# Kernel tuning notes

Hardware: AMD Instinct MI355X
Metric: run time of the kernel (lower is better)

The kernel has to match this reference:

```python
import jax, jax.numpy as jnp
import numpy as np

B, T, N, D = 2, 10, 1024, 1024
NH = 16
HD = D // NH


def setup_inputs() -> dict:
    key = jax.random.key(0)
    ks = jax.random.split(key, 9)
    data = jax.random.normal(ks[0], (B, N, D), jnp.float32)
    traj_pos = jax.random.normal(ks[1], (B, T, N, 3), jnp.float32)
    q = jax.random.normal(ks[2], (B, T, N, 4), jnp.float32)
    traj_quat = q / (jnp.linalg.norm(q, axis=-1, keepdims=True) + 1e-10)
    certainty = jax.random.uniform(ks[3], (B, N), jnp.float32)
    s = 1.0 / np.sqrt(D).astype(np.float32)
    Wq = jax.random.normal(ks[4], (D, D), jnp.float32) * s
    Wk = jax.random.normal(ks[5], (D, D), jnp.float32) * s
    Wv = jax.random.normal(ks[6], (D, D), jnp.float32) * s
    Wo = jax.random.normal(ks[7], (D, D), jnp.float32) * s
    z = jnp.zeros((D,), jnp.float32)
    return {"data": data, "traj_pos": traj_pos, "traj_quat": traj_quat,
            "certainty": certainty, "Wq": Wq, "bq": z, "Wk": Wk, "bk": z,
            "Wv": Wv, "bv": z, "Wo": Wo, "bo": z}


def reference(data, traj_pos, traj_quat, certainty, Wq, bq, Wk, bk, Wv, bv, Wo, bo):
    b, n, d = data.shape
    # --- trajectory similarity scores (same for all batches: torch.mean over batch+time) ---
    # pos_dist[i,j] = mean_{b,t} ||p_bti - p_btj||
    pd = jnp.linalg.norm(traj_pos[:, :, :, None, :] - traj_pos[:, :, None, :, :], axis=-1).mean(axis=(0, 1))  # (n,n)
    qdm = jnp.linalg.norm(traj_quat[:, :, :, None, :] - traj_quat[:, :, None, :, :], axis=-1).mean(axis=(0, 1))
    qdp = jnp.linalg.norm(traj_quat[:, :, :, None, :] + traj_quat[:, :, None, :, :], axis=-1).mean(axis=(0, 1))
    qd = jnp.minimum(qdm, qdp)
    traj = jnp.exp(-pd - qd)
    traj = traj / traj.sum(axis=-1, keepdims=True)  # (n,n) row-normalized

    def proj(x, W, bias):
        return (x @ W.T + bias).reshape(b, n, NH, HD).transpose(0, 2, 1, 3)  # (b,h,n,hd)

    Q = proj(data, Wq, bq)
    K = proj(data, Wk, bk)
    V = proj(data, Wv, bv)
    scores = jnp.einsum('bhid,bhjd->bhij', Q, K) / np.sqrt(HD).astype(np.float32)
    combined = scores + 0.5 * traj[None, None]  # broadcast over (batch, heads)
    attn = jax.nn.softmax(combined, axis=-1)
    out = jnp.einsum('bhij,bhjd->bhid', attn, V).transpose(0, 2, 1, 3).reshape(b, n, d)
    out = out @ Wo.T + bo
    # certainty update from attention entropy
    avg_attn = attn.mean(axis=1)  # (b,n,n)
    p = jnp.clip(avg_attn, 1e-10, None)
    Hent = -jnp.sum(p * jnp.log(p), axis=-1)  # (b,n)
    H_max = np.log(n).astype(np.float32)
    new_certainty = jnp.maximum(certainty, jax.nn.sigmoid(H_max - Hent))
    return out, new_certainty
```

## Files before the change

### kernel.cpp

```cpp
#include <hip/hip_runtime.h>
#include <math.h>

#define NB 2
#define NN 1024
#define DD 1024
#define NHH 16
#define HDD 64
#define BTT 20

typedef unsigned short u16;
typedef short bf16x8 __attribute__((ext_vector_type(8)));
typedef float f32x4 __attribute__((ext_vector_type(4)));

#define HMAXL 6.93147180559945f
#define C1 0.18033688011112042f
#define TLC 0.72134752044448170f
#define KC  0.072134752044448170f
#define CH 520

#define TRAJ_OFF 0
#define TL_OFF    1048576
#define DATAB_OFF 1572864
#define WQB_OFF   2621440
#define WKB_OFF   3145728
#define WVB_OFF   3670016
#define WOB_OFF   4194304
#define QB_OFF    4718592
#define KB_OFF    5767168
#define VT_OFF    6815744
#define AOB_OFF   7864320
#define LV_OFF    8912896
#define HPART_OFF 8945664
#define RSP_OFF   8978432

__device__ __forceinline__ float b2f(u16 h) { return __uint_as_float(((unsigned)h) << 16); }
__device__ __forceinline__ u16 f2bf(float f) {
  unsigned u = __float_as_uint(f);
  return (u16)((u + 0x7fffu + ((u >> 16) & 1u)) >> 16);
}
__device__ __forceinline__ void dma16(const void* g, void* l) {
  __builtin_amdgcn_global_load_lds((const __attribute__((address_space(1))) void*)g,
                                   (__attribute__((address_space(3))) void*)l, 16, 0, 0);
}

__global__ __launch_bounds__(256) void prep_kernel(const float* __restrict__ data,
                                                   const float* __restrict__ w0,
                                                   const float* __restrict__ w1,
                                                   const float* __restrict__ w2,
                                                   const float* __restrict__ w3,
                                                   u16* __restrict__ dd,
                                                   u16* __restrict__ d0, u16* __restrict__ d1,
                                                   u16* __restrict__ d2, u16* __restrict__ d3,
                                                   const float* __restrict__ pos,
                                                   const float* __restrict__ quat,
                                                   float* __restrict__ w,
                                                   float* __restrict__ rsp) {
  const int tid = threadIdx.x;
  const int bid = blockIdx.x;
  __shared__ float ld[8][BTT][8];
  __shared__ float wredS[4][8];
  if (bid >= 512) {
    int cb = bid - 512;
    int z = cb >> 10;
    const float* s;
    u16* d;
    size_t off = 0;
    if (z < 2) { s = data; d = dd; off = (size_t)z * 1048576; }
    else if (z == 2) { s = w0; d = d0; }
    else if (z == 3) { s = w1; d = d1; }
    else if (z == 4) { s = w2; d = d2; }
    else { s = w3; d = d3; }
    size_t i = off + (size_t)((cb & 1023) * 256 + tid) * 4;
    float4 v = *(const float4*)(s + i);
    ushort4 o = {f2bf(v.x), f2bf(v.y), f2bf(v.z), f2bf(v.w)};
    *(ushort4*)(d + i) = o;
    return;
  }
  const int jx = bid & 3;
  const int j = jx * 256 + tid;
  const int i0 = (bid >> 2) * 8;
  if (tid < 8 * BTT) {
    int ii = tid / BTT, bt = tid % BTT;
    const float* pp = pos + ((size_t)bt * NN + i0 + ii) * 3;
    ld[ii][bt][0] = pp[0]; ld[ii][bt][1] = pp[1]; ld[ii][bt][2] = pp[2];
    *(float4*)&ld[ii][bt][4] = *(const float4*)(quat + ((size_t)bt * NN + i0 + ii) * 4);
  }
  __syncthreads();
  float acc[8] = {};
  for (int bt = 0; bt < BTT; ++bt) {
    const float* pj = pos + ((size_t)bt * NN + j) * 3;
    float pjx = pj[0], pjy = pj[1], pjz = pj[2];
    float4 qj = *(const float4*)(quat + ((size_t)bt * NN + j) * 4);
#pragma unroll
    for (int ii = 0; ii < 8; ++ii) {
      float4 pi = *(const float4*)&ld[ii][bt][0];
      float4 qi = *(const float4*)&ld[ii][bt][4];
      float dx = pi.x - pjx, dy = pi.y - pjy, dz = pi.z - pjz;
      float d2 = fmaf(dz, dz, fmaf(dy, dy, dx * dx));
      float dot = fmaf(qi.w, qj.w, fmaf(qi.z, qj.z, fmaf(qi.y, qj.y, qi.x * qj.x)));
      float tq = fmaf(-2.f, fabsf(dot), 2.f);
      acc[ii] += sqrtf(d2) + sqrtf(fmaxf(tq, 0.f));
    }
  }
  const int wv = tid >> 6;
#pragma unroll
  for (int ii = 0; ii < 8; ++ii) {
    float v = exp2f(-acc[ii] * KC);
    w[(size_t)(i0 + ii) * NN + j] = v;
    float s = v;
#pragma unroll
    for (int off = 1; off < 64; off <<= 1) s += __shfl_xor(s, off, 64);
    if ((tid & 63) == 0) wredS[wv][ii] = s;
  }
  __syncthreads();
  if (tid < 8)
    rsp[jx * 1024 + i0 + tid] = wredS[0][tid] + wredS[1][tid] + wredS[2][tid] + wredS[3][tid];
}

__global__ __launch_bounds__(256) void qkv_trajB_kernel(const u16* __restrict__ Ab,
                                                        const u16* __restrict__ Wq,
                                                        const u16* __restrict__ Wk,
                                                        const u16* __restrict__ Wv,
                                                        const float* __restrict__ bq,
                                                        const float* __restrict__ bk,
                                                        const float* __restrict__ bv,
                                                        u16* __restrict__ Qb,
                                                        u16* __restrict__ Kb,
                                                        u16* __restrict__ VtT,
                                                        const float* __restrict__ wtr,
                                                        const float* __restrict__ rsp,
                                                        u16* __restrict__ tl) {
  const int tid = threadIdx.x;
  __shared__ __align__(16) u16 As[128 * 32];
  __shared__ __align__(16) u16 Bs[64 * 32];
  if (blockIdx.x < 256) {
    int base = blockIdx.x * 4;
#pragma unroll
    for (int r = 0; r < 4; ++r) {
      int i = base + r;
      float inv = TLC / (rsp[i] + rsp[1024 + i] + rsp[2048 + i] + rsp[3072 + i]);
      float4 w4 = *(const float4*)(wtr + (size_t)i * NN + tid * 4);
      ushort4 o = {f2bf(w4.x * inv), f2bf(w4.y * inv), f2bf(w4.z * inv), f2bf(w4.w * inv)};
      *(ushort4*)(tl + (size_t)i * NN + tid * 4) = o;
    }
    return;
  }
  const int bid = blockIdx.x - 256;
  const int z = bid >> 8;
  const int rem = bid & 255;
  const int bn = (rem & 15) << 6;
  const int bm = (rem >> 4) << 7;
  const u16* Wb = z == 0 ? Wq : (z == 1 ? Wk : Wv);
  const float* bias = z == 0 ? bq : (z == 1 ? bk : bv);
  const int w = tid >> 6, l = tid & 63, g = l >> 4, ln = l & 15;
  const int srow = w * 16 + (l >> 2);
  const int scol = (l & 3) * 8;
  const u16* Ap0 = Ab + (size_t)(bm + srow) * DD + scol;
  const u16* Ap1 = Ab + (size_t)(bm + 64 + srow) * DD + scol;
  const u16* Bp0 = Wb + (size_t)(bn + srow) * DD + scol;
  u16* dA0 = As + w * 512;
  u16* dA1 = As + 2048 + w * 512;
  u16* dB0 = Bs + w * 512;
  const int mw = (w & 1) * 64, nw = (w >> 1) * 32;
  f32x4 zero4 = {0.f, 0.f, 0.f, 0.f};
  f32x4 acc[4][2];
#pragma unroll
  for (int mt = 0; mt < 4; ++mt)
#pragma unroll
    for (int nt = 0; nt < 2; ++nt) acc[mt][nt] = zero4;
  for (int k0 = 0; k0 < DD; k0 += 32) {
    __syncthreads();
    dma16(Ap0 + k0, dA0); dma16(Ap1 + k0, dA1);
    dma16(Bp0 + k0, dB0);
    __syncthreads();
    bf16x8 bfr[2], afr[4];
#pragma unroll
    for (int nt = 0; nt < 2; ++nt)
      bfr[nt] = *(const bf16x8*)&Bs[(nw + nt * 16 + ln) * 32 + g * 8];
#pragma unroll
    for (int mt = 0; mt < 4; ++mt)
      afr[mt] = *(const bf16x8*)&As[(mw + mt * 16 + ln) * 32 + g * 8];
#pragma unroll
    for (int mt = 0; mt < 4; ++mt)
#pragma unroll
      for (int nt = 0; nt < 2; ++nt)
        acc[mt][nt] = __builtin_amdgcn_mfma_f32_16x16x32_bf16(afr[mt], bfr[nt], acc[mt][nt], 0, 0, 0);
  }
#pragma unroll
  for (int nt = 0; nt < 2; ++nt) {
    int n = bn + nw + nt * 16 + ln;
    float bb = bias[n];
    if (z == 2) {
      int row = (((bm >> 10) << 4) + (n >> 6)) * 64 + (n & 63);
#pragma unroll
      for (int mt = 0; mt < 4; ++mt) {
        int tok = (bm & 1023) + mw + mt * 16 + g * 4;
        ushort4 pk = {f2bf(acc[mt][nt][0] + bb), f2bf(acc[mt][nt][1] + bb),
                      f2bf(acc[mt][nt][2] + bb), f2bf(acc[mt][nt][3] + bb)};
        *(ushort4*)(VtT + (size_t)row * NN + tok) = pk;
      }
    } else {
      u16* outp = z == 0 ? Qb : Kb;
#pragma unroll
      for (int mt = 0; mt < 4; ++mt) {
#pragma unroll
        for (int r = 0; r < 4; ++r) {
          int m = bm + mw + mt * 16 + g * 4 + r;
          outp[(size_t)m * DD + n] = f2bf(acc[mt][nt][r] + bb);
        }
      }
    }
  }
}

__global__ __launch_bounds__(256) void att_kernel(const u16* __restrict__ Qb,
                                                  const u16* __restrict__ Kb,
                                                  const u16* __restrict__ VtT,
                                                  const u16* __restrict__ tl,
                                                  u16* __restrict__ AOb,
                                                  float* __restrict__ Lv) {
  const int tid = threadIdx.x;
  const int bh = blockIdx.y;
  const int b = bh >> 4, h = bh & 15;
  const int i0 = blockIdx.x << 6;
  const int w = tid >> 6, l = tid & 63, g = l >> 4, ln = l & 15;
  const int wi0 = w * 16;
  __shared__ __align__(16) u16 Qs[8 * CH];
  __shared__ __align__(16) u16 Ks[2][8 * CH];
  __shared__ __align__(16) u16 Vts[2][8 * CH];
  __shared__ __align__(16) u16 Pt[64 * 72];
  __shared__ float lsc[64];
  const int c0 = 2 * w, c1 = 2 * w + 1;
  const int rr = 8 * (l >> 3);
  const int dcol = (l & 7) * 8;
  dma16(Qb + ((size_t)(b * NN) + i0 + c0 + rr) * DD + h * HDD + dcol, Qs + c0 * CH);
  dma16(Qb + ((size_t)(b * NN) + i0 + c1 + rr) * DD + h * HDD + dcol, Qs + c1 * CH);
  const int ig = i0 + wi0 + ln;
  const int lnlo = (ln & 7) * CH;
  const int lnhi = (ln >> 3) * 64;
  f32x4 zero4 = {0.f, 0.f, 0.f, 0.f};
  f32x4 oacc[4];
#pragma unroll
  for (int nt = 0; nt < 4; ++nt) oacc[nt] = zero4;
  float lacc = 0.f;
  for (int j0 = 0; j0 < NN; j0 += 128) {
    __syncthreads();
#pragma unroll
    for (int u = 0; u < 2; ++u) {
      int jb = j0 + u * 64;
      dma16(Kb + ((size_t)(b * NN) + jb + c0 + rr) * DD + h * HDD + dcol, Ks[u] + c0 * CH);
      dma16(Kb + ((size_t)(b * NN) + jb + c1 + rr) * DD + h * HDD + dcol, Ks[u] + c1 * CH);
      dma16(VtT + ((size_t)(bh * 64) + c0 + rr) * NN + jb + dcol, Vts[u] + c0 * CH);
      dma16(VtT + ((size_t)(bh * 64) + c1 + rr) * NN + jb + dcol, Vts[u] + c1 * CH);
    }
    ushort4 tlv[2][4];
#pragma unroll
    for (int u = 0; u < 2; ++u)
#pragma unroll
      for (int jt = 0; jt < 4; ++jt)
        tlv[u][jt] = *(const ushort4*)(tl + (size_t)ig * NN + j0 + u * 64 + jt * 16 + g * 4);
    __syncthreads();
    bf16x8 qf[2];
    qf[0] = *(const bf16x8*)&Qs[lnlo + (2 * w) * 64 + lnhi + g * 8];
    qf[1] = *(const bf16x8*)&Qs[lnlo + (2 * w) * 64 + lnhi + 32 + g * 8];
#pragma unroll
    for (int u = 0; u < 2; ++u) {
      f32x4 sacc[4];
      __builtin_amdgcn_s_setprio(1);
#pragma unroll
      for (int jt = 0; jt < 4; ++jt) {
        sacc[jt] = zero4;
#pragma unroll
        for (int kc = 0; kc < 2; ++kc) {
          bf16x8 af = *(const bf16x8*)&Ks[u][lnlo + (2 * jt) * 64 + lnhi + kc * 32 + g * 8];
          sacc[jt] = __builtin_amdgcn_mfma_f32_16x16x32_bf16(af, qf[kc], sacc[jt], 0, 0, 0);
        }
      }
      __builtin_amdgcn_s_setprio(0);
#pragma unroll
      for (int jt = 0; jt < 4; ++jt) {
        float e0 = exp2f(sacc[jt][0] * C1 + b2f(tlv[u][jt].x));
        float e1 = exp2f(sacc[jt][1] * C1 + b2f(tlv[u][jt].y));
        float e2 = exp2f(sacc[jt][2] * C1 + b2f(tlv[u][jt].z));
        float e3 = exp2f(sacc[jt][3] * C1 + b2f(tlv[u][jt].w));
        lacc += (e0 + e1) + (e2 + e3);
        ushort4 pk = {f2bf(e0), f2bf(e1), f2bf(e2), f2bf(e3)};
        *(ushort4*)(Pt + (wi0 + ln) * 72 + jt * 16 + g * 4) = pk;
      }
      bf16x8 pf[2];
      pf[0] = *(const bf16x8*)&Pt[(wi0 + ln) * 72 + g * 8];
      pf[1] = *(const bf16x8*)&Pt[(wi0 + ln) * 72 + 32 + g * 8];
      __builtin_amdgcn_s_setprio(1);
#pragma unroll
      for (int nt = 0; nt < 4; ++nt) {
#pragma unroll
        for (int kc = 0; kc < 2; ++kc) {
          bf16x8 vf = *(const bf16x8*)&Vts[u][lnlo + (2 * nt) * 64 + lnhi + kc * 32 + g * 8];
          oacc[nt] = __builtin_amdgcn_mfma_f32_16x16x32_bf16(pf[kc], vf, oacc[nt], 0, 0, 0);
        }
      }
      __builtin_amdgcn_s_setprio(0);
    }
  }
  lacc += __shfl_xor(lacc, 16, 64);
  lacc += __shfl_xor(lacc, 32, 64);
  if (g == 0) {
    Lv[(size_t)bh * NN + i0 + wi0 + ln] = lacc;
    lsc[wi0 + ln] = 1.f / lacc;
  }
  __syncthreads();
#pragma unroll
  for (int nt = 0; nt < 4; ++nt) {
    int d = nt * 16 + ln;
#pragma unroll
    for (int r = 0; r < 4; ++r) {
      int i = wi0 + g * 4 + r;
      float v = oacc[nt][r] * lsc[i];
      AOb[((size_t)(b * NN) + i0 + i) * DD + h * HDD + d] = f2bf(v);
    }
  }
}

__global__ __launch_bounds__(256) void ent_kernel(const u16* __restrict__ Qb,
                                                  const u16* __restrict__ Kb,
                                                  const u16* __restrict__ tl,
                                                  const float* __restrict__ Lv,
                                                  float* __restrict__ Hp) {
  const int tid = threadIdx.x;
  const int jx = blockIdx.x & 15;
  const int iy = (blockIdx.x >> 4) & 15;
  const int b = blockIdx.x >> 8;
  const int j0 = jx << 6, i0 = iy << 6;
  const int w = tid >> 6, l = tid & 63, g = l >> 4, ln = l & 15;
  const int wi0 = w * 16;
  __shared__ __align__(16) u16 Qs[32 * CH];
  __shared__ __align__(16) u16 Ks[32 * CH];
  __shared__ float linv[NHH * 64];
#pragma unroll
  for (int rep = 0; rep < 4; ++rep) {
    int idx = tid + (rep << 8);
    int hh = idx >> 6, ii = idx & 63;
    linv[hh * 64 + ii] = 1.f / Lv[((size_t)((b << 4) + hh)) * NN + i0 + ii];
  }
  const int rlo = l >> 5;
  const int scol = (l & 31) * 8;
  const int ig = i0 + wi0 + ln;
  const int elo = (ln >> 1) * CH;
  const int ehi = (ln & 1) * 256;
  ushort4 tlv[4];
#pragma unroll
  for (int jt = 0; jt < 4; ++jt)
    tlv[jt] = *(const ushort4*)(tl + (size_t)ig * NN + j0 + jt * 16 + g * 4);
  float P[4][4] = {};
  f32x4 zero4 = {0.f, 0.f, 0.f, 0.f};
  for (int hb = 0; hb < 4; ++hb) {
    __syncthreads();
#pragma unroll
    for (int cc = 0; cc < 8; ++cc) {
      int c = w * 8 + cc;
      dma16(Qb + ((size_t)(b * NN) + i0 + 2 * c + rlo) * DD + hb * 256 + scol, Qs + c * CH);
      dma16(Kb + ((size_t)(b * NN) + j0 + 2 * c + rlo) * DD + hb * 256 + scol, Ks + c * CH);
    }
    __syncthreads();
#pragma unroll
    for (int hl = 0; hl < 4; ++hl) {
      float li = linv[(hb * 4 + hl) * 64 + wi0 + ln];
      bf16x8 qf[2];
      qf[0] = *(const bf16x8*)&Qs[(w * 8) * CH + elo + ehi + hl * 64 + g * 8];
      qf[1] = *(const bf16x8*)&Qs[(w * 8) * CH + elo + ehi + hl * 64 + 32 + g * 8];
#pragma unroll
      for (int jt = 0; jt < 4; ++jt) {
        f32x4 sacc = zero4;
        __builtin_amdgcn_s_setprio(1);
#pragma unroll
        for (int kc = 0; kc < 2; ++kc) {
          bf16x8 af = *(const bf16x8*)&Ks[(jt * 8) * CH + elo + ehi + hl * 64 + kc * 32 + g * 8];
          sacc = __builtin_amdgcn_mfma_f32_16x16x32_bf16(af, qf[kc], sacc, 0, 0, 0);
        }
        __builtin_amdgcn_s_setprio(0);
        P[jt][0] += exp2f(sacc[0] * C1 + b2f(tlv[jt].x)) * li;
        P[jt][1] += exp2f(sacc[1] * C1 + b2f(tlv[jt].y)) * li;
        P[jt][2] += exp2f(sacc[2] * C1 + b2f(tlv[jt].z)) * li;
        P[jt][3] += exp2f(sacc[3] * C1 + b2f(tlv[jt].w)) * li;
      }
    }
  }
  float hs = 0.f;
#pragma unroll
  for (int jt = 0; jt < 4; ++jt) {
#pragma unroll
    for (int r = 0; r < 4; ++r) {
      float p = fmaxf(P[jt][r] * (1.f / NHH), 1e-10f);
      hs -= p * logf(p);
    }
  }
  hs += __shfl_xor(hs, 16, 64);
  hs += __shfl_xor(hs, 32, 64);
  if (g == 0) Hp[jx * 2048 + (size_t)b * NN + i0 + wi0 + ln] = hs;
}

__global__ __launch_bounds__(256) void gemmo_cert_kernel(const u16* __restrict__ Ab,
                                                         const u16* __restrict__ Wb,
                                                         const float* __restrict__ bias,
                                                         float* __restrict__ C,
                                                         const float* __restrict__ Hp,
                                                         const float* __restrict__ cert,
                                                         float* __restrict__ outc) {
  const int tid = threadIdx.x;
  __shared__ __align__(16) u16 As[128 * 32];
  __shared__ __align__(16) u16 Bs[64 * 32];
  if (blockIdx.x >= 256) {
    int idx = (blockIdx.x - 256) * 256 + tid;
    float H = 0.f;
#pragma unroll
    for (int jt = 0; jt < 16; ++jt) H += Hp[jt * 2048 + idx];
    float sg = 1.f / (1.f + expf(H - HMAXL));
    outc[idx] = fmaxf(cert[idx], sg);
    return;
  }
  const int bn = (blockIdx.x & 15) << 6;
  const int bm = (blockIdx.x >> 4) << 7;
  const int w = tid >> 6, l = tid & 63, g = l >> 4, ln = l & 15;
  const int srow = w * 16 + (l >> 2);
  const int scol = (l & 3) * 8;
  const u16* Ap0 = Ab + (size_t)(bm + srow) * DD + scol;
  const u16* Ap1 = Ab + (size_t)(bm + 64 + srow) * DD + scol;
  const u16* Bp0 = Wb + (size_t)(bn + srow) * DD + scol;
  u16* dA0 = As + w * 512;
  u16* dA1 = As + 2048 + w * 512;
  u16* dB0 = Bs + w * 512;
  const int mw = (w & 1) * 64, nw = (w >> 1) * 32;
  f32x4 zero4 = {0.f, 0.f, 0.f, 0.f};
  f32x4 acc[4][2];
#pragma unroll
  for (int mt = 0; mt < 4; ++mt)
#pragma unroll
    for (int nt = 0; nt < 2; ++nt) acc[mt][nt] = zero4;
  for (int k0 = 0; k0 < DD; k0 += 32) {
    __syncthreads();
    dma16(Ap0 + k0, dA0); dma16(Ap1 + k0, dA1);
    dma16(Bp0 + k0, dB0);
    __syncthreads();
    bf16x8 bfr[2], afr[4];
#pragma unroll
    for (int nt = 0; nt < 2; ++nt)
      bfr[nt] = *(const bf16x8*)&Bs[(nw + nt * 16 + ln) * 32 + g * 8];
#pragma unroll
    for (int mt = 0; mt < 4; ++mt)
      afr[mt] = *(const bf16x8*)&As[(mw + mt * 16 + ln) * 32 + g * 8];
#pragma unroll
    for (int mt = 0; mt < 4; ++mt)
#pragma unroll
      for (int nt = 0; nt < 2; ++nt)
        acc[mt][nt] = __builtin_amdgcn_mfma_f32_16x16x32_bf16(afr[mt], bfr[nt], acc[mt][nt], 0, 0, 0);
  }
#pragma unroll
  for (int nt = 0; nt < 2; ++nt) {
    int n = bn + nw + nt * 16 + ln;
    float bb = bias[n];
#pragma unroll
    for (int mt = 0; mt < 4; ++mt) {
#pragma unroll
      for (int r = 0; r < 4; ++r) {
        int m = bm + mw + mt * 16 + g * 4 + r;
        C[(size_t)m * DD + n] = acc[mt][nt][r] + bb;
      }
    }
  }
}

extern "C" void kernel_launch(void* const* d_in, const int* in_sizes, int n_in,
                              void* d_out, int out_size, void* d_ws, size_t ws_size,
                              hipStream_t stream) {
  const float* data      = (const float*)d_in[0];
  const float* traj_pos  = (const float*)d_in[1];
  const float* traj_quat = (const float*)d_in[2];
  const float* certainty = (const float*)d_in[3];
  const float* Wq = (const float*)d_in[4];
  const float* bq = (const float*)d_in[5];
  const float* Wk = (const float*)d_in[6];
  const float* bk = (const float*)d_in[7];
  const float* Wv = (const float*)d_in[8];
  const float* bv = (const float*)d_in[9];
  const float* Wo = (const float*)d_in[10];
  const float* bo = (const float*)d_in[11];

  float* ws = (float*)d_ws;
  float* wtr  = ws + TRAJ_OFF;
  u16* tl    = (u16*)(ws + TL_OFF);
  u16* datab = (u16*)(ws + DATAB_OFF);
  u16* wqb   = (u16*)(ws + WQB_OFF);
  u16* wkb   = (u16*)(ws + WKB_OFF);
  u16* wvb   = (u16*)(ws + WVB_OFF);
  u16* wob   = (u16*)(ws + WOB_OFF);
  u16* Qb    = (u16*)(ws + QB_OFF);
  u16* Kb    = (u16*)(ws + KB_OFF);
  u16* VtT   = (u16*)(ws + VT_OFF);
  u16* AOb   = (u16*)(ws + AOB_OFF);
  float* Lv   = ws + LV_OFF;
  float* Hp   = ws + HPART_OFF;
  float* rsp  = ws + RSP_OFF;
  float* out  = (float*)d_out;
  float* outc = out + (size_t)NB * NN * DD;

  prep_kernel<<<6656, 256, 0, stream>>>(data, Wq, Wk, Wv, Wo,
                                        datab, wqb, wkb, wvb, wob,
                                        traj_pos, traj_quat, wtr, rsp);
  qkv_trajB_kernel<<<1024, 256, 0, stream>>>(datab, wqb, wkb, wvb, bq, bk, bv,
                                             Qb, Kb, VtT, wtr, rsp, tl);
  att_kernel<<<dim3(NN / 64, NB * NHH), 256, 0, stream>>>(Qb, Kb, VtT, tl, AOb, Lv);
  ent_kernel<<<512, 256, 0, stream>>>(Qb, Kb, tl, Lv, Hp);
  gemmo_cert_kernel<<<264, 256, 0, stream>>>(AOb, wob, bo, out, Hp, certainty, outc);
}
```

Before: 207.1 us.

## Store attention exponentials in global memory and compute entropy in the output GEMM kernel

The attention kernel now also writes each head's unnormalised bf16 exp scores into a large global buffer. This replaces the separate entropy kernel, which recomputed QK^T and the exponentials for every head. The entropy reduction moves into extra blocks of the output-projection kernel, which read those values back, scale them by 1/L per head, average over heads and reduce per row. The aim is to drop the redundant matmul and exp work and one kernel launch. The cost is about 64 MB of extra global writes and reads, plus a larger workspace requirement.

```diff
diff --git a/kernel.cpp b/kernel.cpp
--- a/kernel.cpp
+++ b/kernel.cpp
@@ -13,6 +13,7 @@
 typedef float f32x4 __attribute__((ext_vector_type(4)));
 
 #define HMAXL 6.93147180559945f
+#define LN2 0.69314718055994531f
 #define C1 0.18033688011112042f
 #define TLC 0.72134752044448170f
 #define KC  0.072134752044448170f
@@ -30,8 +31,8 @@
 #define VT_OFF    6815744
 #define AOB_OFF   7864320
 #define LV_OFF    8912896
-#define HPART_OFF 8945664
 #define RSP_OFF   8978432
+#define EB_OFF    8982528
 
 __device__ __forceinline__ float b2f(u16 h) { return __uint_as_float(((unsigned)h) << 16); }
 __device__ __forceinline__ u16 f2bf(float f) {
@@ -218,7 +219,8 @@
                                                   const u16* __restrict__ VtT,
                                                   const u16* __restrict__ tl,
                                                   u16* __restrict__ AOb,
-                                                  float* __restrict__ Lv) {
+                                                  float* __restrict__ Lv,
+                                                  u16* __restrict__ Eb) {
   const int tid = threadIdx.x;
   const int bh = blockIdx.y;
   const int b = bh >> 4, h = bh & 15;
@@ -236,6 +238,7 @@
   dma16(Qb + ((size_t)(b * NN) + i0 + c0 + rr) * DD + h * HDD + dcol, Qs + c0 * CH);
   dma16(Qb + ((size_t)(b * NN) + i0 + c1 + rr) * DD + h * HDD + dcol, Qs + c1 * CH);
   const int ig = i0 + wi0 + ln;
+  u16* Erow = Eb + ((size_t)bh * NN + ig) * NN;
   const int lnlo = (ln & 7) * CH;
   const int lnhi = (ln >> 3) * 64;
   f32x4 zero4 = {0.f, 0.f, 0.f, 0.f};
@@ -286,6 +289,7 @@
         lacc += (e0 + e1) + (e2 + e3);
         ushort4 pk = {f2bf(e0), f2bf(e1), f2bf(e2), f2bf(e3)};
         *(ushort4*)(Pt + (wi0 + ln) * 72 + jt * 16 + g * 4) = pk;
+        *(ushort4*)(Erow + j0 + u * 64 + jt * 16 + g * 4) = pk;
       }
       bf16x8 pf[2];
       pf[0] = *(const bf16x8*)&Pt[(wi0 + ln) * 72 + g * 8];
@@ -321,101 +325,62 @@
   }
 }
 
-__global__ __launch_bounds__(256) void ent_kernel(const u16* __restrict__ Qb,
-                                                  const u16* __restrict__ Kb,
-                                                  const u16* __restrict__ tl,
-                                                  const float* __restrict__ Lv,
-                                                  float* __restrict__ Hp) {
-  const int tid = threadIdx.x;
-  const int jx = blockIdx.x & 15;
-  const int iy = (blockIdx.x >> 4) & 15;
-  const int b = blockIdx.x >> 8;
-  const int j0 = jx << 6, i0 = iy << 6;
-  const int w = tid >> 6, l = tid & 63, g = l >> 4, ln = l & 15;
-  const int wi0 = w * 16;
-  __shared__ __align__(16) u16 Qs[32 * CH];
-  __shared__ __align__(16) u16 Ks[32 * CH];
-  __shared__ float linv[NHH * 64];
-#pragma unroll
-  for (int rep = 0; rep < 4; ++rep) {
-    int idx = tid + (rep << 8);
-    int hh = idx >> 6, ii = idx & 63;
-    linv[hh * 64 + ii] = 1.f / Lv[((size_t)((b << 4) + hh)) * NN + i0 + ii];
-  }
-  const int rlo = l >> 5;
-  const int scol = (l & 31) * 8;
-  const int ig = i0 + wi0 + ln;
-  const int elo = (ln >> 1) * CH;
-  const int ehi = (ln & 1) * 256;
-  ushort4 tlv[4];
-#pragma unroll
-  for (int jt = 0; jt < 4; ++jt)
-    tlv[jt] = *(const ushort4*)(tl + (size_t)ig * NN + j0 + jt * 16 + g * 4);
-  float P[4][4] = {};
-  f32x4 zero4 = {0.f, 0.f, 0.f, 0.f};
-  for (int hb = 0; hb < 4; ++hb) {
-    __syncthreads();
-#pragma unroll
-    for (int cc = 0; cc < 8; ++cc) {
-      int c = w * 8 + cc;
-      dma16(Qb + ((size_t)(b * NN) + i0 + 2 * c + rlo) * DD + hb * 256 + scol, Qs + c * CH);
-      dma16(Kb + ((size_t)(b * NN) + j0 + 2 * c + rlo) * DD + hb * 256 + scol, Ks + c * CH);
-    }
-    __syncthreads();
-#pragma unroll
-    for (int hl = 0; hl < 4; ++hl) {
-      float li = linv[(hb * 4 + hl) * 64 + wi0 + ln];
-      bf16x8 qf[2];
-      qf[0] = *(const bf16x8*)&Qs[(w * 8) * CH + elo + ehi + hl * 64 + g * 8];
-      qf[1] = *(const bf16x8*)&Qs[(w * 8) * CH + elo + ehi + hl * 64 + 32 + g * 8];
-#pragma unroll
-      for (int jt = 0; jt < 4; ++jt) {
-        f32x4 sacc = zero4;
-        __builtin_amdgcn_s_setprio(1);
-#pragma unroll
-        for (int kc = 0; kc < 2; ++kc) {
-          bf16x8 af = *(const bf16x8*)&Ks[(jt * 8) * CH + elo + ehi + hl * 64 + kc * 32 + g * 8];
-          sacc = __builtin_amdgcn_mfma_f32_16x16x32_bf16(af, qf[kc], sacc, 0, 0, 0);
-        }
-        __builtin_amdgcn_s_setprio(0);
-        P[jt][0] += exp2f(sacc[0] * C1 + b2f(tlv[jt].x)) * li;
-        P[jt][1] += exp2f(sacc[1] * C1 + b2f(tlv[jt].y)) * li;
-        P[jt][2] += exp2f(sacc[2] * C1 + b2f(tlv[jt].z)) * li;
-        P[jt][3] += exp2f(sacc[3] * C1 + b2f(tlv[jt].w)) * li;
-      }
-    }
-  }
-  float hs = 0.f;
-#pragma unroll
-  for (int jt = 0; jt < 4; ++jt) {
-#pragma unroll
-    for (int r = 0; r < 4; ++r) {
-      float p = fmaxf(P[jt][r] * (1.f / NHH), 1e-10f);
-      hs -= p * logf(p);
-    }
-  }
-  hs += __shfl_xor(hs, 16, 64);
-  hs += __shfl_xor(hs, 32, 64);
-  if (g == 0) Hp[jx * 2048 + (size_t)b * NN + i0 + wi0 + ln] = hs;
-}
-
-__global__ __launch_bounds__(256) void gemmo_cert_kernel(const u16* __restrict__ Ab,
-                                                         const u16* __restrict__ Wb,
-                                                         const float* __restrict__ bias,
-                                                         float* __restrict__ C,
-                                                         const float* __restrict__ Hp,
-                                                         const float* __restrict__ cert,
-                                                         float* __restrict__ outc) {
+__global__ __launch_bounds__(256) void gemmo_ent_kernel(const u16* __restrict__ Ab,
+                                                        const u16* __restrict__ Wb,
+                                                        const float* __restrict__ bias,
+                                                        float* __restrict__ C,
+                                                        const u16* __restrict__ Eb,
+                                                        const float* __restrict__ Lv,
+                                                        const float* __restrict__ cert,
+                                                        float* __restrict__ outc) {
   const int tid = threadIdx.x;
   __shared__ __align__(16) u16 As[128 * 32];
   __shared__ __align__(16) u16 Bs[64 * 32];
+  __shared__ float linvS[4][16];
+  __shared__ float redS[4][4];
   if (blockIdx.x >= 256) {
-    int idx = (blockIdx.x - 256) * 256 + tid;
-    float H = 0.f;
-#pragma unroll
-    for (int jt = 0; jt < 16; ++jt) H += Hp[jt * 2048 + idx];
-    float sg = 1.f / (1.f + expf(H - HMAXL));
-    outc[idx] = fmaxf(cert[idx], sg);
+    const int e = blockIdx.x - 256;
+    const int b = e >> 8;
+    const int ib4 = (e & 255) << 2;
+    if (tid < 64) {
+      int r = tid >> 4, h = tid & 15;
+      linvS[r][h] = 1.f / Lv[((size_t)(b * 16 + h)) * NN + ib4 + r];
+    }
+    __syncthreads();
+    const int jb = tid * 4;
+    float A[4];
+#pragma unroll
+    for (int r = 0; r < 4; ++r) {
+      float s0 = 0.f, s1 = 0.f, s2 = 0.f, s3 = 0.f;
+#pragma unroll
+      for (int h = 0; h < 16; ++h) {
+        ushort4 v = *(const ushort4*)(Eb + (((size_t)(b * 16 + h)) * NN + ib4 + r) * NN + jb);
+        float li = linvS[r][h];
+        s0 = fmaf(b2f(v.x), li, s0); s1 = fmaf(b2f(v.y), li, s1);
+        s2 = fmaf(b2f(v.z), li, s2); s3 = fmaf(b2f(v.w), li, s3);
+      }
+      float p0 = fmaxf(s0 * (1.f / NHH), 1e-10f);
+      float p1 = fmaxf(s1 * (1.f / NHH), 1e-10f);
+      float p2 = fmaxf(s2 * (1.f / NHH), 1e-10f);
+      float p3 = fmaxf(s3 * (1.f / NHH), 1e-10f);
+      A[r] = p0 * __log2f(p0) + p1 * __log2f(p1) + p2 * __log2f(p2) + p3 * __log2f(p3);
+    }
+#pragma unroll
+    for (int r = 0; r < 4; ++r)
+#pragma unroll
+      for (int off = 1; off < 64; off <<= 1) A[r] += __shfl_xor(A[r], off, 64);
+    const int wv = tid >> 6;
+    if ((tid & 63) == 0) {
+#pragma unroll
+      for (int r = 0; r < 4; ++r) redS[wv][r] = A[r];
+    }
+    __syncthreads();
+    if (tid < 4) {
+      float H = -LN2 * (redS[0][tid] + redS[1][tid] + redS[2][tid] + redS[3][tid]);
+      int idx = b * NN + ib4 + tid;
+      float sg = 1.f / (1.f + expf(H - HMAXL));
+      outc[idx] = fmaxf(cert[idx], sg);
+    }
     return;
   }
   const int bn = (blockIdx.x & 15) << 6;
@@ -498,8 +463,8 @@
   u16* VtT   = (u16*)(ws + VT_OFF);
   u16* AOb   = (u16*)(ws + AOB_OFF);
   float* Lv   = ws + LV_OFF;
-  float* Hp   = ws + HPART_OFF;
   float* rsp  = ws + RSP_OFF;
+  u16* Eb    = (u16*)(ws + EB_OFF);
   float* out  = (float*)d_out;
   float* outc = out + (size_t)NB * NN * DD;
 
@@ -508,7 +473,6 @@
                                         traj_pos, traj_quat, wtr, rsp);
   qkv_trajB_kernel<<<1024, 256, 0, stream>>>(datab, wqb, wkb, wvb, bq, bk, bv,
                                              Qb, Kb, VtT, wtr, rsp, tl);
-  att_kernel<<<dim3(NN / 64, NB * NHH), 256, 0, stream>>>(Qb, Kb, VtT, tl, AOb, Lv);
-  ent_kernel<<<512, 256, 0, stream>>>(Qb, Kb, tl, Lv, Hp);
-  gemmo_cert_kernel<<<264, 256, 0, stream>>>(AOb, wob, bo, out, Hp, certainty, outc);
-}
+  att_kernel<<<dim3(NN / 64, NB * NHH), 256, 0, stream>>>(Qb, Kb, VtT, tl, AOb, Lv, Eb);
+  gemmo_ent_kernel<<<768, 256, 0, stream>>>(AOb, wob, bo, out, Eb, Lv, certainty, outc);
+}
```

New measurement: 198.9 us. -3.9%, faster.
